# Kernel tuning notes

Measured on AMD Instinct MI355X. Metric: run time of the kernel, lower is better.

## Reference

```python
import jax, jax.numpy as jnp
import numpy as np

B, S, D = 2, 2048, 1024   # batch, seq, token_dim
H, E = 16, 64             # heads, embedding_size per head


def setup_inputs() -> dict:
    key = jax.random.key(0)
    ks = jax.random.split(key, 5)
    x = jax.random.normal(ks[0], (B, S, D), dtype=jnp.float32)
    attention_mask = jnp.ones((B, S), dtype=jnp.int32)  # accepted but unused, as in source
    # torch.rand -> uniform [0,1)
    w_queries = jax.random.uniform(ks[1], (H, D, E), dtype=jnp.float32)
    w_keys = jax.random.uniform(ks[2], (H, D, E), dtype=jnp.float32)
    w_values = jax.random.uniform(ks[3], (H, D, E), dtype=jnp.float32)
    w_agg = jax.random.uniform(ks[4], (H * E, D), dtype=jnp.float32)
    return {"x": x, "attention_mask": attention_mask, "w_queries": w_queries,
            "w_keys": w_keys, "w_values": w_values, "w_agg": w_agg}


def reference(x, attention_mask, w_queries, w_keys, w_values, w_agg):
    # Batched over all heads at once (original loops in Python per head).
    q = jnp.einsum('bsd,hde->bhse', x, w_queries)  # [B,H,S,E]
    k = jnp.einsum('bsd,hde->bhse', x, w_keys)
    v = jnp.einsum('bsd,hde->bhse', x, w_values)
    scores = jnp.einsum('bhse,bhte->bhst', q, k) / jnp.sqrt(jnp.float32(E))  # [B,H,S,S]
    # NOTE: source applies softmax over dim=1 of the per-head [B,S,S] scores,
    # i.e. over the QUERY axis (axis=2 here), not the usual key axis.
    attn = jax.nn.softmax(scores, axis=2)
    heads = jnp.einsum('bhst,bhte->bhse', attn, v)  # [B,H,S,E]
    # concat along last dim in head order -> [B,S,H*E]
    multi = jnp.transpose(heads, (0, 2, 1, 3)).reshape(B, S, H * E)
    return multi @ w_agg  # [B,S,D]
```

## Files before the change

### kernel.cpp

```cpp
#include <hip/hip_runtime.h>
#include <hip/hip_bf16.h>


typedef __attribute__((ext_vector_type(8))) short bf16x8;
typedef __attribute__((ext_vector_type(4))) float f32x4;

#define C1 0.18033688011112042f

__device__ __forceinline__ unsigned short f2bf(float f){
  union { __hip_bfloat16 h; unsigned short u; } cv;
  cv.h = __float2bfloat16(f);
  return cv.u;
}
__device__ __forceinline__ unsigned int pk2(float a, float b){
  union { __hip_bfloat162 h; unsigned int u; } cv;
  cv.h = __float22bfloat162_rn(make_float2(a, b));
  return cv.u;
}
__device__ __forceinline__ unsigned long long pack4(float a, float b, float c, float d){
  return (unsigned long long)pk2(a, b) | ((unsigned long long)pk2(c, d) << 32);
}
__device__ __forceinline__ float bf2f(unsigned short u){
  unsigned int x = ((unsigned int)u) << 16;
  return __builtin_bit_cast(float, x);
}

__device__ __forceinline__ void swap32(unsigned a, unsigned b, unsigned &x, unsigned &y){
#if __has_builtin(__builtin_amdgcn_permlane32_swap)
  auto r = __builtin_amdgcn_permlane32_swap(a, b, false, false);
  x = r[0]; y = r[1];
#else
  int lane = threadIdx.x & 63;
  unsigned as = __shfl_xor((int)a, 32), bs = __shfl_xor((int)b, 32);
  x = (lane & 32) ? bs : a;
  y = (lane & 32) ? b : as;
#endif
}
__device__ __forceinline__ void swap16(unsigned a, unsigned b, unsigned &x, unsigned &y){
#if __has_builtin(__builtin_amdgcn_permlane16_swap)
  auto r = __builtin_amdgcn_permlane16_swap(a, b, false, false);
  x = r[0]; y = r[1];
#else
  int lane = threadIdx.x & 63;
  unsigned as = __shfl_xor((int)a, 16), bs = __shfl_xor((int)b, 16);
  x = (lane & 16) ? bs : a;
  y = (lane & 16) ? b : as;
#endif
}

#define GLOAD16(SRC, DST)                                                        \
  __builtin_amdgcn_global_load_lds(                                              \
      (const __attribute__((address_space(1))) void*)(SRC),                      \
      (__attribute__((address_space(3))) void*)(DST), 16, 0, 0)

__global__ void k_cvt_x(const float* __restrict__ in, unsigned short* __restrict__ out){
  int i = (blockIdx.x * 256 + threadIdx.x) * 4;
  float4 v = *reinterpret_cast<const float4*>(in + i);
  *reinterpret_cast<unsigned long long*>(out + i) = pack4(v.x, v.y, v.z, v.w);
}

__global__ __launch_bounds__(256) void k_cvt_w3t(const float* __restrict__ wq,
                                                 const float* __restrict__ wk,
                                                 const float* __restrict__ wv,
                                                 unsigned short* __restrict__ out){
  __shared__ unsigned short T[64][72];
  const int z = blockIdx.z;
  const float* w = ((z == 0) ? wq : ((z == 1) ? wk : wv)) + ((size_t)blockIdx.y << 16);
  const int d0 = blockIdx.x * 64;
  const int r = threadIdx.x >> 2, c0 = (threadIdx.x & 3) << 4;
  const float* src = w + ((size_t)(d0 + r) << 6) + c0;
#pragma unroll
  for (int i = 0; i < 4; ++i){
    float4 v = *(const float4*)(src + 4 * i);
    T[r][c0 + 4 * i + 0] = f2bf(v.x);
    T[r][c0 + 4 * i + 1] = f2bf(v.y);
    T[r][c0 + 4 * i + 2] = f2bf(v.z);
    T[r][c0 + 4 * i + 3] = f2bf(v.w);
  }
  __syncthreads();
  const int e = threadIdx.x >> 2, k0 = (threadIdx.x & 3) << 4;
  union { unsigned short s[8]; bf16x8 v; } u0, u1;
#pragma unroll
  for (int k = 0; k < 8; ++k){ u0.s[k] = T[k0 + k][e]; u1.s[k] = T[k0 + 8 + k][e]; }
  unsigned short* dst = out + ((size_t)z << 20) + (((size_t)blockIdx.y * 64 + e) << 10) + d0 + k0;
  *(bf16x8*)dst = u0.v;
  *(bf16x8*)(dst + 8) = u1.v;
}

__global__ __launch_bounds__(256) void k_cvt_waggt(const float* __restrict__ w,
                                                   unsigned short* __restrict__ out){
  __shared__ unsigned short T[64][72];
  const int d0 = blockIdx.x * 64, he0 = blockIdx.y * 64;
  const int r = threadIdx.x >> 2, c0 = (threadIdx.x & 3) << 4;
  const float* src = w + ((size_t)(he0 + r) << 10) + d0 + c0;
#pragma unroll
  for (int i = 0; i < 4; ++i){
    float4 v = *(const float4*)(src + 4 * i);
    T[r][c0 + 4 * i + 0] = f2bf(v.x);
    T[r][c0 + 4 * i + 1] = f2bf(v.y);
    T[r][c0 + 4 * i + 2] = f2bf(v.z);
    T[r][c0 + 4 * i + 3] = f2bf(v.w);
  }
  __syncthreads();
  const int d = threadIdx.x >> 2, k0 = (threadIdx.x & 3) << 4;
  union { unsigned short s[8]; bf16x8 v; } u0, u1;
#pragma unroll
  for (int k = 0; k < 8; ++k){ u0.s[k] = T[k0 + k][d]; u1.s[k] = T[k0 + 8 + k][d]; }
  unsigned short* dst = out + ((size_t)(d0 + d) << 11) + he0 + k0;
  *(bf16x8*)dst = u0.v;
  *(bf16x8*)(dst + 8) = u1.v;
  *(bf16x8*)(dst + 1024) = u0.v;
  *(bf16x8*)(dst + 1032) = u1.v;
}

__global__ __launch_bounds__(256) void k_proj(const unsigned short* __restrict__ Wall,
                                              const unsigned short* __restrict__ Xb,
                                              unsigned short* __restrict__ Qb,
                                              unsigned short* __restrict__ Kb,
                                              unsigned short* __restrict__ Vt){
  __shared__ __align__(16) unsigned short lds[2][2][4096];
  const int z = blockIdx.z;
  const unsigned short* Wt = Wall + ((size_t)z << 20);
  const int t = threadIdx.x;
  const int w = t >> 6, lane = t & 63, g = lane >> 4, cl = lane & 15;
  const int wn = w >> 1, wm = w & 1;
  const int n0 = blockIdx.x * 128, m0 = blockIdx.y * 128;

  const int rowS = t & 127;
  const unsigned short* sA = Wt + (size_t)(n0 + rowS) * 1024 + (t >> 7) * 8;
  const unsigned short* sB = Xb + (size_t)(m0 + rowS) * 1024 + (t >> 7) * 8;

  f32x4 acc[4][4];
#pragma unroll
  for (int i = 0; i < 4; ++i)
#pragma unroll
    for (int j = 0; j < 4; ++j) acc[i][j] = f32x4{0.f, 0.f, 0.f, 0.f};

  GLOAD16(sA,      &lds[0][0][t * 8]);
  GLOAD16(sA + 16, &lds[0][0][t * 8 + 2048]);
  GLOAD16(sB,      &lds[0][1][t * 8]);
  GLOAD16(sB + 16, &lds[0][1][t * 8 + 2048]);
  __syncthreads();

#pragma unroll 2
  for (int kt = 0; kt < 32; ++kt){
    const int cur = kt & 1;
    if (kt < 31){
      const unsigned short* nA = sA + (kt + 1) * 32;
      const unsigned short* nB = sB + (kt + 1) * 32;
      GLOAD16(nA,      &lds[cur ^ 1][0][t * 8]);
      GLOAD16(nA + 16, &lds[cur ^ 1][0][t * 8 + 2048]);
      GLOAD16(nB,      &lds[cur ^ 1][1][t * 8]);
      GLOAD16(nB + 16, &lds[cur ^ 1][1][t * 8 + 2048]);
    }
    const unsigned short* la = &lds[cur][0][g * 1024];
    const unsigned short* lb = &lds[cur][1][g * 1024];
    bf16x8 af[4], bq[4];
#pragma unroll
    for (int i = 0; i < 4; ++i) af[i] = *(const bf16x8*)(la + (wn * 64 + i * 16 + cl) * 8);
#pragma unroll
    for (int j = 0; j < 4; ++j) bq[j] = *(const bf16x8*)(lb + (wm * 64 + j * 16 + cl) * 8);
#pragma unroll
    for (int i = 0; i < 4; ++i)
#pragma unroll
      for (int j = 0; j < 4; ++j)
        acc[i][j] = __builtin_amdgcn_mfma_f32_16x16x32_bf16(af[i], bq[j], acc[i][j], 0, 0, 0);
    __syncthreads();
  }

  const float scale = (z == 0) ? C1 : 1.f;
#pragma unroll
  for (int i = 0; i < 4; ++i)
#pragma unroll
    for (int j = 0; j < 4; ++j)
#pragma unroll
      for (int jj = 0; jj < 4; ++jj) acc[i][j][jj] *= scale;

  if (z < 2){
    unsigned short* outp = (z == 0) ? Qb : Kb;
#pragma unroll
    for (int i = 0; i < 4; ++i)
#pragma unroll
      for (int j = 0; j < 4; ++j){
        int m = m0 + wm * 64 + 16 * j + cl;
        int n = n0 + wn * 64 + 16 * i + 4 * g;
        *reinterpret_cast<unsigned long long*>(outp + (size_t)m * 1024 + n) =
            pack4(acc[i][j][0], acc[i][j][1], acc[i][j][2], acc[i][j][3]);
      }
  } else {
    int b = m0 >> 11;
#pragma unroll
    for (int i = 0; i < 4; ++i)
#pragma unroll
      for (int j = 0; j < 4; ++j){
        int c2 = (m0 & 2047) + wm * 64 + 16 * j + cl;
        int nb = b * 1024 + n0 + wn * 64 + 16 * i + 4 * g;
#pragma unroll
        for (int jj = 0; jj < 4; ++jj)
          Vt[(size_t)(nb + jj) * 2048 + c2] = f2bf(acc[i][j][jj]);
      }
  }
}

__global__ __launch_bounds__(256) void k_agg(const unsigned short* __restrict__ Wa,
                                             const unsigned short* __restrict__ Hd,
                                             float* __restrict__ outp){
  __shared__ __align__(16) unsigned short lds[2][2][4096];
  const int t = threadIdx.x;
  const int w = t >> 6, lane = t & 63, g = lane >> 4, cl = lane & 15;
  const int wn = w >> 1, wm = w & 1;
  const int n0 = blockIdx.x * 128, m0 = blockIdx.y * 128;

  const int rowS = t & 127;
  const unsigned short* sA = Wa + (size_t)(n0 + rowS) * 2048 + (t >> 7) * 8;
  const unsigned short* sB = Hd + (size_t)(m0 + rowS) * 2048 + (t >> 7) * 8;

  f32x4 acc[4][4];
#pragma unroll
  for (int i = 0; i < 4; ++i)
#pragma unroll
    for (int j = 0; j < 4; ++j) acc[i][j] = f32x4{0.f, 0.f, 0.f, 0.f};

  GLOAD16(sA,      &lds[0][0][t * 8]);
  GLOAD16(sA + 16, &lds[0][0][t * 8 + 2048]);
  GLOAD16(sB,      &lds[0][1][t * 8]);
  GLOAD16(sB + 16, &lds[0][1][t * 8 + 2048]);
  __syncthreads();

#pragma unroll 2
  for (int kt = 0; kt < 64; ++kt){
    const int cur = kt & 1;
    if (kt < 63){
      const unsigned short* nA = sA + (kt + 1) * 32;
      const unsigned short* nB = sB + (kt + 1) * 32;
      GLOAD16(nA,      &lds[cur ^ 1][0][t * 8]);
      GLOAD16(nA + 16, &lds[cur ^ 1][0][t * 8 + 2048]);
      GLOAD16(nB,      &lds[cur ^ 1][1][t * 8]);
      GLOAD16(nB + 16, &lds[cur ^ 1][1][t * 8 + 2048]);
    }
    const unsigned short* la = &lds[cur][0][g * 1024];
    const unsigned short* lb = &lds[cur][1][g * 1024];
    bf16x8 af[4], bq[4];
#pragma unroll
    for (int i = 0; i < 4; ++i) af[i] = *(const bf16x8*)(la + (wn * 64 + i * 16 + cl) * 8);
#pragma unroll
    for (int j = 0; j < 4; ++j) bq[j] = *(const bf16x8*)(lb + (wm * 64 + j * 16 + cl) * 8);
#pragma unroll
    for (int i = 0; i < 4; ++i)
#pragma unroll
      for (int j = 0; j < 4; ++j)
        acc[i][j] = __builtin_amdgcn_mfma_f32_16x16x32_bf16(af[i], bq[j], acc[i][j], 0, 0, 0);
    __syncthreads();
  }
#pragma unroll
  for (int i = 0; i < 4; ++i)
#pragma unroll
    for (int j = 0; j < 4; ++j){
      int m = m0 + wm * 64 + 16 * j + cl;
      int n = n0 + wn * 64 + 16 * i + 4 * g;
      *reinterpret_cast<f32x4*>(outp + (size_t)m * 1024 + n) = acc[i][j];
    }
}

__global__ __launch_bounds__(256, 4) void k_stats(const unsigned short* __restrict__ Qb,
                                                  const unsigned short* __restrict__ Kb,
                                                  float* __restrict__ mp,
                                                  float* __restrict__ lp){
  __shared__ __align__(16) unsigned short Qs[2][64][64];
  const int B = blockIdx.x;
  const int xcd = B & 7, rest = B >> 3;
  const int tx = rest & 7, gi = rest >> 3;
  const int grp = xcd + 8 * gi;
  const int bh = grp & 31, z = grp >> 5;
  const int b = bh >> 4, h = bh & 15;
  const int w = threadIdx.x >> 6, lane = threadIdx.x & 63;
  const int g = lane >> 4, cl = lane & 15;
  const int t0 = tx * 256 + w * 64;

  const unsigned short* kp = Kb + (size_t)(b * 2048 + t0 + cl) * 1024 + h * 64 + g * 8;
  bf16x8 a[4][2];
#pragma unroll
  for (int ti = 0; ti < 4; ++ti){
    a[ti][0] = *(const bf16x8*)(kp + (size_t)ti * 16 * 1024);
    a[ti][1] = *(const bf16x8*)(kp + (size_t)ti * 16 * 1024 + 32);
  }

  const int r0 = threadIdx.x >> 3, sl = threadIdx.x & 7;
  const unsigned short* qsrc = Qb + (size_t)(b * 2048 + z * 512 + r0) * 1024 + h * 64
                               + ((sl ^ (r0 & 7)) * 8);
  unsigned short* qdst0 = &Qs[0][0][0] + threadIdx.x * 8;

  const int e0 = (g ^ (cl & 7)) * 8;
  const int e1 = ((g + 4) ^ (cl & 7)) * 8;

  float m[16], l[16];
#pragma unroll
  for (int i = 0; i < 16; ++i){ m[i] = -3.0e38f; l[i] = 0.f; }

  GLOAD16(qsrc,             qdst0);
  GLOAD16(qsrc + 32 * 1024, qdst0 + 2048);
  __syncthreads();
  for (int c = 0; c < 8; ++c){
    const int buf = c & 1;
    if (c < 7){
      const unsigned short* s2 = qsrc + (size_t)(c + 1) * 64 * 1024;
      unsigned short* d2 = qdst0 + (buf ^ 1) * 4096;
      GLOAD16(s2,             d2);
      GLOAD16(s2 + 32 * 1024, d2 + 2048);
    }
#pragma unroll
    for (int st = 0; st < 4; ++st){
      const unsigned short* qrow = &Qs[buf][st * 16 + cl][0];
      bf16x8 b0 = *(const bf16x8*)(qrow + e0);
      bf16x8 b1 = *(const bf16x8*)(qrow + e1);
#pragma unroll
      for (int ti = 0; ti < 4; ++ti){
        f32x4 zz = {0.f, 0.f, 0.f, 0.f};
        f32x4 d = __builtin_amdgcn_mfma_f32_16x16x32_bf16(a[ti][0], b0, zz, 0, 0, 0);
        d = __builtin_amdgcn_mfma_f32_16x16x32_bf16(a[ti][1], b1, d, 0, 0, 0);
#pragma unroll
        for (int j = 0; j < 4; ++j) m[ti * 4 + j] = fmaxf(m[ti * 4 + j], d[j]);
      }
    }
    __syncthreads();
  }
#pragma unroll
  for (int off = 1; off < 16; off <<= 1)
#pragma unroll
    for (int i = 0; i < 16; ++i) m[i] = fmaxf(m[i], __shfl_xor(m[i], off));

  GLOAD16(qsrc,             qdst0);
  GLOAD16(qsrc + 32 * 1024, qdst0 + 2048);
  __syncthreads();
  for (int c = 0; c < 8; ++c){
    const int buf = c & 1;
    if (c < 7){
      const unsigned short* s2 = qsrc + (size_t)(c + 1) * 64 * 1024;
      unsigned short* d2 = qdst0 + (buf ^ 1) * 4096;
      GLOAD16(s2,             d2);
      GLOAD16(s2 + 32 * 1024, d2 + 2048);
    }
#pragma unroll
    for (int st = 0; st < 4; ++st){
      const unsigned short* qrow = &Qs[buf][st * 16 + cl][0];
      bf16x8 b0 = *(const bf16x8*)(qrow + e0);
      bf16x8 b1 = *(const bf16x8*)(qrow + e1);
#pragma unroll
      for (int ti = 0; ti < 4; ++ti){
        f32x4 zz = {0.f, 0.f, 0.f, 0.f};
        f32x4 d = __builtin_amdgcn_mfma_f32_16x16x32_bf16(a[ti][0], b0, zz, 0, 0, 0);
        d = __builtin_amdgcn_mfma_f32_16x16x32_bf16(a[ti][1], b1, d, 0, 0, 0);
#pragma unroll
        for (int j = 0; j < 4; ++j) l[ti * 4 + j] += exp2f(d[j] - m[ti * 4 + j]);
      }
    }
    __syncthreads();
  }
#pragma unroll
  for (int off = 1; off < 16; off <<= 1)
#pragma unroll
    for (int i = 0; i < 16; ++i) l[i] += __shfl_xor(l[i], off);

  if (cl == 0){
    size_t base = ((size_t)z * 32 + bh) * 2048 + t0;
#pragma unroll
    for (int ti = 0; ti < 4; ++ti){
      f32x4 mv = {m[ti * 4 + 0], m[ti * 4 + 1], m[ti * 4 + 2], m[ti * 4 + 3]};
      f32x4 lv = {l[ti * 4 + 0], l[ti * 4 + 1], l[ti * 4 + 2], l[ti * 4 + 3]};
      *(f32x4*)(mp + base + ti * 16 + 4 * g) = mv;
      *(f32x4*)(lp + base + ti * 16 + 4 * g) = lv;
    }
  }
}

__global__ void k_mcomb(const float* __restrict__ mp, const float* __restrict__ lp,
                        float* __restrict__ m2, float* __restrict__ rl){
  int i = blockIdx.x * 256 + threadIdx.x;
  float m0 = mp[i], m1 = mp[65536 + i], m2v = mp[131072 + i], m3 = mp[196608 + i];
  float l0 = lp[i], l1 = lp[65536 + i], l2 = lp[131072 + i], l3 = lp[196608 + i];
  float m = fmaxf(fmaxf(m0, m1), fmaxf(m2v, m3));
  float l = l0 * exp2f(m0 - m) + l1 * exp2f(m1 - m)
          + l2 * exp2f(m2v - m) + l3 * exp2f(m3 - m);
  m2[i] = m;
  rl[i] = 1.f / l;
}

__global__ void k_scale_v(unsigned short* __restrict__ Vt, const float* __restrict__ rl){
  int row = blockIdx.x;
  int b = row >> 10, h = (row >> 6) & 15;
  int t = threadIdx.x * 8;
  const float* r = rl + (size_t)(b * 16 + h) * 2048 + t;
  unsigned short* p = Vt + (size_t)row * 2048 + t;
  bf16x8 v = *(const bf16x8*)p;
  f32x4 r0 = *(const f32x4*)r;
  f32x4 r1 = *(const f32x4*)(r + 4);
  float f[8];
#pragma unroll
  for (int j = 0; j < 8; ++j) f[j] = bf2f((unsigned short)v[j]);
#pragma unroll
  for (int j = 0; j < 4; ++j){ f[j] *= r0[j]; f[4 + j] *= r1[j]; }
  unsigned long long* q = (unsigned long long*)p;
  q[0] = pack4(f[0], f[1], f[2], f[3]);
  q[1] = pack4(f[4], f[5], f[6], f[7]);
}

__global__ __launch_bounds__(256, 4) void k_attn(const unsigned short* __restrict__ Qb,
                                                 const unsigned short* __restrict__ Kb,
                                                 const unsigned short* __restrict__ Vt,
                                                 const float* __restrict__ m2,
                                                 unsigned short* __restrict__ Hd){
  __shared__ __align__(16) unsigned short KsL[2 * 64 * 64];
  __shared__ __align__(16) unsigned short VsL[2 * 64 * 64];
  const int B = blockIdx.x;
  const int xcd = B & 7, rest = B >> 3;
  const int sx = rest & 15, gi = rest >> 4;
  const int grp = xcd + 8 * gi;
  const int bh = grp & 31, z = grp >> 5;
  const int b = bh >> 4, h = bh & 15;
  const int lane = threadIdx.x & 63;
  const int g = lane >> 4, cl = lane & 15;
  const int s0w = sx * 128 + (threadIdx.x >> 6) * 32;
  const int tbase = z * 1024;

  bf16x8 q[2][2];
#pragma unroll
  for (int ss = 0; ss < 2; ++ss){
    const unsigned short* qp = Qb + (size_t)(b * 2048 + s0w + ss * 16 + cl) * 1024 + h * 64 + g * 8;
    q[ss][0] = *(const bf16x8*)(qp);
    q[ss][1] = *(const bf16x8*)(qp + 32);
  }
  f32x4 acc[4][2];
#pragma unroll
  for (int i = 0; i < 4; ++i)
#pragma unroll
    for (int ss = 0; ss < 2; ++ss) acc[i][ss] = f32x4{0.f, 0.f, 0.f, 0.f};

  const int srow = threadIdx.x >> 3;
  const int sseg = ((threadIdx.x & 7) ^ (srow & 7)) * 8;
  const unsigned short* kStage = Kb + (size_t)(b * 2048 + tbase + srow) * 1024 + h * 64 + sseg;
  const unsigned short* vStage = Vt + (size_t)(b * 1024 + h * 64 + srow) * 2048 + tbase + sseg;
  unsigned short* kDst = &KsL[0] + threadIdx.x * 8;
  unsigned short* vDst = &VsL[0] + threadIdx.x * 8;

  const float* mb = m2 + (size_t)bh * 2048 + tbase + 4 * g;
  const int eK = (g ^ (cl & 7)) * 8;
  const int eK2 = ((g + 4) ^ (cl & 7)) * 8;

#define ASTAGE(c, buf) {                                                          \
    const unsigned short* ks_ = kStage + (size_t)(c) * 64 * 1024;                 \
    const unsigned short* vs_ = vStage + (c) * 64;                                \
    unsigned short* kd_ = kDst + (buf) * 4096;                                    \
    unsigned short* vd_ = vDst + (buf) * 4096;                                    \
    GLOAD16(ks_,             kd_);                                                \
    GLOAD16(ks_ + 32 * 1024, kd_ + 2048);                                         \
    GLOAD16(vs_,             vd_);                                                \
    GLOAD16(vs_ + (size_t)32 * 2048, vd_ + 2048); }

  ASTAGE(0, 0);
  __syncthreads();

  for (int c = 0; c < 16; ++c){
    const int buf = c & 1;
    if (c < 15) ASTAGE(c + 1, buf ^ 1);
    const unsigned short* Kbuf = &KsL[0] + buf * 4096;
    const unsigned short* Vbuf = &VsL[0] + buf * 4096;
#pragma unroll
    for (int sc = 0; sc < 2; ++sc){
      const unsigned short* kr0 = Kbuf + (sc * 32 + cl) * 64;
      const unsigned short* kr1 = Kbuf + (sc * 32 + 16 + cl) * 64;
      bf16x8 a00 = *(const bf16x8*)(kr0 + eK);
      bf16x8 a01 = *(const bf16x8*)(kr0 + eK2);
      bf16x8 a10 = *(const bf16x8*)(kr1 + eK);
      bf16x8 a11 = *(const bf16x8*)(kr1 + eK2);
      f32x4 mv0 = *(const f32x4*)(mb + c * 64 + sc * 32);
      f32x4 mv1 = *(const f32x4*)(mb + c * 64 + sc * 32 + 16);

      bf16x8 pb[2];
#pragma unroll
      for (int ss = 0; ss < 2; ++ss){
        f32x4 zz = {0.f, 0.f, 0.f, 0.f};
        f32x4 d0 = __builtin_amdgcn_mfma_f32_16x16x32_bf16(a00, q[ss][0], zz, 0, 0, 0);
        d0 = __builtin_amdgcn_mfma_f32_16x16x32_bf16(a01, q[ss][1], d0, 0, 0, 0);
        f32x4 d1 = __builtin_amdgcn_mfma_f32_16x16x32_bf16(a10, q[ss][0], zz, 0, 0, 0);
        d1 = __builtin_amdgcn_mfma_f32_16x16x32_bf16(a11, q[ss][1], d1, 0, 0, 0);
        unsigned w00 = pk2(exp2f(d0[0] - mv0[0]), exp2f(d0[1] - mv0[1]));
        unsigned w01 = pk2(exp2f(d0[2] - mv0[2]), exp2f(d0[3] - mv0[3]));
        unsigned w10 = pk2(exp2f(d1[0] - mv1[0]), exp2f(d1[1] - mv1[1]));
        unsigned w11 = pk2(exp2f(d1[2] - mv1[2]), exp2f(d1[3] - mv1[3]));
        unsigned sa0, sb0, sa1, sb1, W0, W1, W2, W3;
        swap32(w00, w10, sa0, sb0);
        swap32(w01, w11, sa1, sb1);
        swap16(sa0, sb0, W0, W2);
        swap16(sa1, sb1, W1, W3);
        union { unsigned u[4]; bf16x8 v; } fr;
        fr.u[0] = W0; fr.u[1] = W1; fr.u[2] = W2; fr.u[3] = W3;
        pb[ss] = fr.v;
      }
#pragma unroll
      for (int i = 0; i < 4; ++i){
        bf16x8 av = *(const bf16x8*)(Vbuf + (16 * i + cl) * 64 + ((sc * 4 + g) ^ (cl & 7)) * 8);
        acc[i][0] = __builtin_amdgcn_mfma_f32_16x16x32_bf16(av, pb[0], acc[i][0], 0, 0, 0);
        acc[i][1] = __builtin_amdgcn_mfma_f32_16x16x32_bf16(av, pb[1], acc[i][1], 0, 0, 0);
      }
    }
    __syncthreads();
  }
#undef ASTAGE
#pragma unroll
  for (int i = 0; i < 4; ++i)
#pragma unroll
    for (int ss = 0; ss < 2; ++ss){
      *reinterpret_cast<unsigned long long*>(
          Hd + (size_t)(b * 2048 + s0w + ss * 16 + cl) * 2048 + z * 1024 + h * 64 + 16 * i + 4 * g) =
          pack4(acc[i][ss][0], acc[i][ss][1], acc[i][ss][2], acc[i][ss][3]);
    }
}

extern "C" void kernel_launch(void* const* d_in, const int* in_sizes, int n_in,
                              void* d_out, int out_size, void* d_ws, size_t ws_size,
                              hipStream_t stream) {
  const float* x    = (const float*)d_in[0];
  const float* wq   = (const float*)d_in[2];
  const float* wk   = (const float*)d_in[3];
  const float* wv   = (const float*)d_in[4];
  const float* wagg = (const float*)d_in[5];
  float* outp = (float*)d_out;

  char* ws = (char*)d_ws;
  unsigned short* Xb  = (unsigned short*)(ws);
  unsigned short* Hd  = (unsigned short*)(ws);
  unsigned short* Wall= (unsigned short*)(ws + 16777216);
  float* mp = (float*)(ws + 16777216);
  float* lp = (float*)(ws + 17825792);
  float* m2 = (float*)(ws + 18874368);
  float* rl = (float*)(ws + 19136512);
  unsigned short* Wat = (unsigned short*)(ws + 23068672);
  unsigned short* Qb  = (unsigned short*)(ws + 27262976);
  unsigned short* Kb  = (unsigned short*)(ws + 35651584);
  unsigned short* Vt  = (unsigned short*)(ws + 44040192);

  k_cvt_x    <<<dim3(4096),       dim3(256), 0, stream>>>(x, Xb);
  k_cvt_w3t  <<<dim3(16, 16, 3),  dim3(256), 0, stream>>>(wq, wk, wv, Wall);
  k_cvt_waggt<<<dim3(16, 16),     dim3(256), 0, stream>>>(wagg, Wat);

  k_proj<<<dim3(8, 32, 3), dim3(256), 0, stream>>>(Wall, Xb, Qb, Kb, Vt);

  k_stats  <<<dim3(1024), dim3(256), 0, stream>>>(Qb, Kb, mp, lp);
  k_mcomb  <<<dim3(256),  dim3(256), 0, stream>>>(mp, lp, m2, rl);
  k_scale_v<<<dim3(2048), dim3(256), 0, stream>>>(Vt, rl);

  k_attn<<<dim3(1024), dim3(256), 0, stream>>>(Qb, Kb, Vt, m2, Hd);
  k_agg <<<dim3(8, 32), dim3(256), 0, stream>>>(Wat, Hd, outp);
}
```

Before: 251.1 us.

## Use online softmax stats in one pass, split queries 8-way, stage max in LDS

The stats kernel now computes the running max and sum in a single pass with an online-softmax update, instead of two passes over Q. It also splits the query range into 8 chunks, using twice the blocks to recover parallelism, and merges partials with a rescaled shuffle reduction. k_mcomb combines 8 partials. k_attn preloads the per-key max into LDS and raises wave priority around its MFMA sections. The costs are extra exp per score in stats, a larger mp/lp workspace, and more partial data to combine.

```diff
diff --git a/kernel.cpp b/kernel.cpp
--- a/kernel.cpp
+++ b/kernel.cpp
@@ -286,7 +286,7 @@
   }
 
   const int r0 = threadIdx.x >> 3, sl = threadIdx.x & 7;
-  const unsigned short* qsrc = Qb + (size_t)(b * 2048 + z * 512 + r0) * 1024 + h * 64
+  const unsigned short* qsrc = Qb + (size_t)(b * 2048 + z * 256 + r0) * 1024 + h * 64
                                + ((sl ^ (r0 & 7)) * 8);
   unsigned short* qdst0 = &Qs[0][0][0] + threadIdx.x * 8;
 
@@ -300,9 +300,9 @@
   GLOAD16(qsrc,             qdst0);
   GLOAD16(qsrc + 32 * 1024, qdst0 + 2048);
   __syncthreads();
-  for (int c = 0; c < 8; ++c){
+  for (int c = 0; c < 4; ++c){
     const int buf = c & 1;
-    if (c < 7){
+    if (c < 3){
       const unsigned short* s2 = qsrc + (size_t)(c + 1) * 64 * 1024;
       unsigned short* d2 = qdst0 + (buf ^ 1) * 4096;
       GLOAD16(s2,             d2);
@@ -319,48 +319,29 @@
         f32x4 d = __builtin_amdgcn_mfma_f32_16x16x32_bf16(a[ti][0], b0, zz, 0, 0, 0);
         d = __builtin_amdgcn_mfma_f32_16x16x32_bf16(a[ti][1], b1, d, 0, 0, 0);
 #pragma unroll
-        for (int j = 0; j < 4; ++j) m[ti * 4 + j] = fmaxf(m[ti * 4 + j], d[j]);
+        for (int j = 0; j < 4; ++j){
+          int idx = ti * 4 + j;
+          float dlt = d[j] - m[idx];
+          float e = exp2f(-fabsf(dlt));
+          bool gt = dlt > 0.f;
+          l[idx] = gt ? fmaf(l[idx], e, 1.f) : (l[idx] + e);
+          m[idx] = gt ? d[j] : m[idx];
+        }
       }
     }
     __syncthreads();
   }
 #pragma unroll
-  for (int off = 1; off < 16; off <<= 1)
-#pragma unroll
-    for (int i = 0; i < 16; ++i) m[i] = fmaxf(m[i], __shfl_xor(m[i], off));
-
-  GLOAD16(qsrc,             qdst0);
-  GLOAD16(qsrc + 32 * 1024, qdst0 + 2048);
-  __syncthreads();
-  for (int c = 0; c < 8; ++c){
-    const int buf = c & 1;
-    if (c < 7){
-      const unsigned short* s2 = qsrc + (size_t)(c + 1) * 64 * 1024;
-      unsigned short* d2 = qdst0 + (buf ^ 1) * 4096;
-      GLOAD16(s2,             d2);
-      GLOAD16(s2 + 32 * 1024, d2 + 2048);
-    }
-#pragma unroll
-    for (int st = 0; st < 4; ++st){
-      const unsigned short* qrow = &Qs[buf][st * 16 + cl][0];
-      bf16x8 b0 = *(const bf16x8*)(qrow + e0);
-      bf16x8 b1 = *(const bf16x8*)(qrow + e1);
-#pragma unroll
-      for (int ti = 0; ti < 4; ++ti){
-        f32x4 zz = {0.f, 0.f, 0.f, 0.f};
-        f32x4 d = __builtin_amdgcn_mfma_f32_16x16x32_bf16(a[ti][0], b0, zz, 0, 0, 0);
-        d = __builtin_amdgcn_mfma_f32_16x16x32_bf16(a[ti][1], b1, d, 0, 0, 0);
-#pragma unroll
-        for (int j = 0; j < 4; ++j) l[ti * 4 + j] += exp2f(d[j] - m[ti * 4 + j]);
-      }
-    }
-    __syncthreads();
-  }
-#pragma unroll
-  for (int off = 1; off < 16; off <<= 1)
-#pragma unroll
-    for (int i = 0; i < 16; ++i) l[i] += __shfl_xor(l[i], off);
-
+  for (int off = 1; off < 16; off <<= 1){
+#pragma unroll
+    for (int i = 0; i < 16; ++i){
+      float om = __shfl_xor(m[i], off);
+      float ol = __shfl_xor(l[i], off);
+      float mn = fmaxf(m[i], om);
+      l[i] = l[i] * exp2f(m[i] - mn) + ol * exp2f(om - mn);
+      m[i] = mn;
+    }
+  }
   if (cl == 0){
     size_t base = ((size_t)z * 32 + bh) * 2048 + t0;
 #pragma unroll
@@ -376,12 +357,13 @@
 __global__ void k_mcomb(const float* __restrict__ mp, const float* __restrict__ lp,
                         float* __restrict__ m2, float* __restrict__ rl){
   int i = blockIdx.x * 256 + threadIdx.x;
-  float m0 = mp[i], m1 = mp[65536 + i], m2v = mp[131072 + i], m3 = mp[196608 + i];
-  float l0 = lp[i], l1 = lp[65536 + i], l2 = lp[131072 + i], l3 = lp[196608 + i];
-  float m = fmaxf(fmaxf(m0, m1), fmaxf(m2v, m3));
-  float l = l0 * exp2f(m0 - m) + l1 * exp2f(m1 - m)
-          + l2 * exp2f(m2v - m) + l3 * exp2f(m3 - m);
-  m2[i] = m;
+  float mm = -3.0e38f;
+#pragma unroll
+  for (int k = 0; k < 8; ++k) mm = fmaxf(mm, mp[i + k * 65536]);
+  float l = 0.f;
+#pragma unroll
+  for (int k = 0; k < 8; ++k) l += lp[i + k * 65536] * exp2f(mp[i + k * 65536] - mm);
+  m2[i] = mm;
   rl[i] = 1.f / l;
 }
 
@@ -411,6 +393,7 @@
                                                  unsigned short* __restrict__ Hd){
   __shared__ __align__(16) unsigned short KsL[2 * 64 * 64];
   __shared__ __align__(16) unsigned short VsL[2 * 64 * 64];
+  __shared__ __align__(16) float Ms[1024];
   const int B = blockIdx.x;
   const int xcd = B & 7, rest = B >> 3;
   const int sx = rest & 15, gi = rest >> 4;
@@ -422,6 +405,11 @@
   const int s0w = sx * 128 + (threadIdx.x >> 6) * 32;
   const int tbase = z * 1024;
 
+  {
+    int i = threadIdx.x * 4;
+    *(f32x4*)&Ms[i] = *(const f32x4*)(m2 + (size_t)bh * 2048 + tbase + i);
+  }
+
   bf16x8 q[2][2];
 #pragma unroll
   for (int ss = 0; ss < 2; ++ss){
@@ -442,7 +430,6 @@
   unsigned short* kDst = &KsL[0] + threadIdx.x * 8;
   unsigned short* vDst = &VsL[0] + threadIdx.x * 8;
 
-  const float* mb = m2 + (size_t)bh * 2048 + tbase + 4 * g;
   const int eK = (g ^ (cl & 7)) * 8;
   const int eK2 = ((g + 4) ^ (cl & 7)) * 8;
 
@@ -472,17 +459,19 @@
       bf16x8 a01 = *(const bf16x8*)(kr0 + eK2);
       bf16x8 a10 = *(const bf16x8*)(kr1 + eK);
       bf16x8 a11 = *(const bf16x8*)(kr1 + eK2);
-      f32x4 mv0 = *(const f32x4*)(mb + c * 64 + sc * 32);
-      f32x4 mv1 = *(const f32x4*)(mb + c * 64 + sc * 32 + 16);
+      f32x4 mv0 = *(const f32x4*)&Ms[c * 64 + sc * 32 + 4 * g];
+      f32x4 mv1 = *(const f32x4*)&Ms[c * 64 + sc * 32 + 16 + 4 * g];
 
       bf16x8 pb[2];
 #pragma unroll
       for (int ss = 0; ss < 2; ++ss){
         f32x4 zz = {0.f, 0.f, 0.f, 0.f};
+        __builtin_amdgcn_s_setprio(1);
         f32x4 d0 = __builtin_amdgcn_mfma_f32_16x16x32_bf16(a00, q[ss][0], zz, 0, 0, 0);
         d0 = __builtin_amdgcn_mfma_f32_16x16x32_bf16(a01, q[ss][1], d0, 0, 0, 0);
         f32x4 d1 = __builtin_amdgcn_mfma_f32_16x16x32_bf16(a10, q[ss][0], zz, 0, 0, 0);
         d1 = __builtin_amdgcn_mfma_f32_16x16x32_bf16(a11, q[ss][1], d1, 0, 0, 0);
+        __builtin_amdgcn_s_setprio(0);
         unsigned w00 = pk2(exp2f(d0[0] - mv0[0]), exp2f(d0[1] - mv0[1]));
         unsigned w01 = pk2(exp2f(d0[2] - mv0[2]), exp2f(d0[3] - mv0[3]));
         unsigned w10 = pk2(exp2f(d1[0] - mv1[0]), exp2f(d1[1] - mv1[1]));
@@ -496,12 +485,14 @@
         fr.u[0] = W0; fr.u[1] = W1; fr.u[2] = W2; fr.u[3] = W3;
         pb[ss] = fr.v;
       }
+      __builtin_amdgcn_s_setprio(1);
 #pragma unroll
       for (int i = 0; i < 4; ++i){
         bf16x8 av = *(const bf16x8*)(Vbuf + (16 * i + cl) * 64 + ((sc * 4 + g) ^ (cl & 7)) * 8);
         acc[i][0] = __builtin_amdgcn_mfma_f32_16x16x32_bf16(av, pb[0], acc[i][0], 0, 0, 0);
         acc[i][1] = __builtin_amdgcn_mfma_f32_16x16x32_bf16(av, pb[1], acc[i][1], 0, 0, 0);
       }
+      __builtin_amdgcn_s_setprio(0);
     }
     __syncthreads();
   }
@@ -531,9 +522,9 @@
   unsigned short* Hd  = (unsigned short*)(ws);
   unsigned short* Wall= (unsigned short*)(ws + 16777216);
   float* mp = (float*)(ws + 16777216);
-  float* lp = (float*)(ws + 17825792);
-  float* m2 = (float*)(ws + 18874368);
-  float* rl = (float*)(ws + 19136512);
+  float* lp = (float*)(ws + 18874368);
+  float* m2 = (float*)(ws + 20971520);
+  float* rl = (float*)(ws + 21233664);
   unsigned short* Wat = (unsigned short*)(ws + 23068672);
   unsigned short* Qb  = (unsigned short*)(ws + 27262976);
   unsigned short* Kb  = (unsigned short*)(ws + 35651584);
@@ -545,7 +536,7 @@
 
   k_proj<<<dim3(8, 32, 3), dim3(256), 0, stream>>>(Wall, Xb, Qb, Kb, Vt);
 
-  k_stats  <<<dim3(1024), dim3(256), 0, stream>>>(Qb, Kb, mp, lp);
+  k_stats  <<<dim3(2048), dim3(256), 0, stream>>>(Qb, Kb, mp, lp);
   k_mcomb  <<<dim3(256),  dim3(256), 0, stream>>>(mp, lp, m2, rl);
   k_scale_v<<<dim3(2048), dim3(256), 0, stream>>>(Vt, rl);
 
```

Measured after the change: 289.6 us. 15.3% more time.
